# Kernel optimization log

Hardware: AMD Instinct MI355X
Metric: run time of the kernel (lower is better)

The kernel has to match this reference:

```python
import jax, jax.numpy as jnp
import numpy as np

B, S, D, H = 4, 1024, 1024, 16
HD = D // H
EPS = 1e-5


def layer_norm(x, scale, shift):
    mean = jnp.mean(x, axis=-1, keepdims=True)
    var = jnp.mean((x - mean) ** 2, axis=-1, keepdims=True)
    return scale * (x - mean) / jnp.sqrt(var + EPS) + shift


def gelu_tanh(x):
    c = jnp.sqrt(jnp.asarray(2.0 / jnp.pi, dtype=x.dtype))
    return 0.5 * x * (1.0 + jnp.tanh(c * (x + 0.044715 * x ** 3)))


def setup_inputs() -> dict:
    key = jax.random.key(0)
    ks = jax.random.split(key, 12)
    s = 0.02
    return {
        "x": jax.random.normal(ks[0], (B, S, D), dtype=jnp.float32),
        "attention_mask": jnp.ones((B, S), dtype=jnp.int32),
        "wq": jax.random.normal(ks[1], (D, D), dtype=jnp.float32) * s,
        "wk": jax.random.normal(ks[2], (D, D), dtype=jnp.float32) * s,
        "wv": jax.random.normal(ks[3], (D, D), dtype=jnp.float32) * s,
        "wo": jax.random.normal(ks[4], (D, D), dtype=jnp.float32) * s,
        "bo": jnp.zeros((D,), dtype=jnp.float32),
        "ln1_scale": jnp.ones((D,), dtype=jnp.float32),
        "ln1_shift": jnp.zeros((D,), dtype=jnp.float32),
        "ln2_scale": jnp.ones((D,), dtype=jnp.float32),
        "ln2_shift": jnp.zeros((D,), dtype=jnp.float32),
        "w1": jax.random.normal(ks[5], (D, 4 * D), dtype=jnp.float32) * s,
        "b1": jnp.zeros((4 * D,), dtype=jnp.float32),
        "w2": jax.random.normal(ks[6], (4 * D, D), dtype=jnp.float32) * s,
        "b2": jnp.zeros((D,), dtype=jnp.float32),
    }


def reference(x, attention_mask, wq, wk, wv, wo, bo, ln1_scale, ln1_shift,
              ln2_scale, ln2_shift, w1, b1, w2, b2):
    b, s, d = x.shape
    # --- pre-norm attention ---
    shortcut = x
    h = layer_norm(x, ln1_scale, ln1_shift)
    q = (h @ wq).reshape(b, s, H, HD).transpose(0, 2, 1, 3)  # bhsd
    k = (h @ wk).reshape(b, s, H, HD).transpose(0, 2, 1, 3)
    v = (h @ wv).reshape(b, s, H, HD).transpose(0, 2, 1, 3)
    scores = jnp.einsum('bhqd,bhkd->bhqk', q, k)
    causal = jnp.triu(jnp.ones((s, s), dtype=bool), k=1)  # True above diag -> masked
    neg_inf = jnp.asarray(-jnp.inf, dtype=scores.dtype)
    scores = jnp.where(causal, neg_inf, scores)
    pad = attention_mask[:, None, None, :].astype(bool)  # (b,1,1,k)
    scores = jnp.where(pad, scores, neg_inf)
    attn = jax.nn.softmax(scores / jnp.sqrt(jnp.asarray(HD, dtype=scores.dtype)), axis=-1)
    ctx = jnp.einsum('bhqk,bhkd->bhqd', attn, v)
    ctx = ctx.transpose(0, 2, 1, 3).reshape(b, s, d)
    x = shortcut + (ctx @ wo + bo)
    # --- pre-norm FFN ---
    shortcut = x
    h = layer_norm(x, ln2_scale, ln2_shift)
    h = gelu_tanh(h @ w1 + b1) @ w2 + b2
    return shortcut + h
```

## Files before the change

kernel.cpp:

```cpp
#include <hip/hip_runtime.h>
#include <hip/hip_bf16.h>
#include <math.h>

#define B_ 4
#define S_ 1024
#define D_ 1024
#define H_ 16
#define HD_ 64

typedef __hip_bfloat16 bf16_t;
typedef __attribute__((ext_vector_type(8))) short bf16x8;
typedef __attribute__((ext_vector_type(4))) float floatx4;

__device__ __forceinline__ float bf2f(ushort u) {
  return __uint_as_float((unsigned)u << 16);
}

__global__ __launch_bounds__(256) void prep_kernel(
    const float* __restrict__ x, const float* __restrict__ ln1s,
    const float* __restrict__ ln1b, bf16_t* __restrict__ h,
    const float* __restrict__ wq, const float* __restrict__ wk,
    const float* __restrict__ wv, const float* __restrict__ wo,
    const float* __restrict__ w1, const float* __restrict__ w2,
    bf16_t* __restrict__ wqkv_t, bf16_t* __restrict__ wo_t,
    bf16_t* __restrict__ w1_t, bf16_t* __restrict__ w2_t) {
  const int id = blockIdx.x;
  if (id < 4096) {
    const int row = id;
    float4 v = ((const float4*)(x + (size_t)row * D_))[threadIdx.x];
    float s = v.x + v.y + v.z + v.w;
    float ss = v.x * v.x + v.y * v.y + v.z * v.z + v.w * v.w;
#pragma unroll
    for (int off = 32; off > 0; off >>= 1) {
      s += __shfl_xor(s, off);
      ss += __shfl_xor(ss, off);
    }
    __shared__ float ls[4], lss[4], stats[2];
    const int wave = threadIdx.x >> 6, lane = threadIdx.x & 63;
    if (lane == 0) { ls[wave] = s; lss[wave] = ss; }
    __syncthreads();
    if (threadIdx.x == 0) {
      float t = ls[0] + ls[1] + ls[2] + ls[3];
      float tt = lss[0] + lss[1] + lss[2] + lss[3];
      float mean = t * (1.0f / D_);
      stats[0] = mean;
      stats[1] = rsqrtf(tt * (1.0f / D_) - mean * mean + 1e-5f);
    }
    __syncthreads();
    const float mean = stats[0], rstd = stats[1];
    float4 sc = ((const float4*)ln1s)[threadIdx.x];
    float4 sh = ((const float4*)ln1b)[threadIdx.x];
    bf16_t ob[4];
    ob[0] = __float2bfloat16(sc.x * (v.x - mean) * rstd + sh.x);
    ob[1] = __float2bfloat16(sc.y * (v.y - mean) * rstd + sh.y);
    ob[2] = __float2bfloat16(sc.z * (v.z - mean) * rstd + sh.z);
    ob[3] = __float2bfloat16(sc.w * (v.w - mean) * rstd + sh.w);
    *(ushort4*)(h + (size_t)row * D_ + threadIdx.x * 4) = *(ushort4*)ob;
    return;
  }
  const float* W;
  bf16_t* Wt;
  int K, N, n0, k0;
  if (id < 8192) {
    const int t = id - 4096, which = t >> 10, tile = t & 1023;
    n0 = (tile & 31) * 32;
    k0 = (tile >> 5) * 32;
    K = 1024; N = 1024;
    W = which == 0 ? wq : which == 1 ? wk : which == 2 ? wv : wo;
    Wt = which < 3 ? wqkv_t + (size_t)which * 1024 * 1024 : wo_t;
  } else if (id < 12288) {
    const int tile = id - 8192;
    n0 = (tile & 127) * 32;
    k0 = (tile >> 7) * 32;
    K = 1024; N = 4096;
    W = w1; Wt = w1_t;
  } else {
    const int tile = id - 12288;
    n0 = (tile & 31) * 32;
    k0 = (tile >> 5) * 32;
    K = 4096; N = 1024;
    W = w2; Wt = w2_t;
  }
  __shared__ float t[32][33];
  const int lx = threadIdx.x & 31, ly = threadIdx.x >> 5;
#pragma unroll
  for (int r = ly; r < 32; r += 8) t[r][lx] = W[(size_t)(k0 + r) * N + n0 + lx];
  __syncthreads();
#pragma unroll
  for (int r = ly; r < 32; r += 8)
    Wt[(size_t)(n0 + r) * K + k0 + lx] = __float2bfloat16(t[lx][r]);
}

__global__ __launch_bounds__(256) void mgemm_kernel(const bf16_t* __restrict__ A,
                                                    const bf16_t* __restrict__ Bt,
                                                    const float* __restrict__ bias,
                                                    void* __restrict__ C,
                                                    int M, int N, int K, int Kc,
                                                    int Mt, int Nt, int PM,
                                                    int mode) {
  __shared__ bf16_t As[128 * 64];
  __shared__ bf16_t Bs[128 * 64];
  const int tid = threadIdx.x;
  const int lane = tid & 63, w = tid >> 6;

  const int flat = blockIdx.x;
  const int xcd = flat & 7;
  int t0 = flat >> 3;
  const int mb = xcd % PM, nb = xcd / PM;
  const int mt = mb * Mt + (t0 % Mt);
  t0 /= Mt;
  const int nt = nb * Nt + (t0 % Nt);
  const int z = t0 / Nt;
  const int m0 = mt * 128, n0 = nt * 128;
  const int kz0 = z * Kc;
  const int wm = (w >> 1) * 64, wn = (w & 1) * 64;

  floatx4 zero = {0.f, 0.f, 0.f, 0.f};
  floatx4 acc[4][4];
#pragma unroll
  for (int i = 0; i < 4; i++)
#pragma unroll
    for (int j = 0; j < 4; j++) acc[i][j] = zero;

  const int ro8 = lane >> 3;
  const int g8 = ((lane & 7) ^ ro8) * 8;
  const bf16_t* ga[4];
  const bf16_t* gb[4];
  bf16_t* la[4];
  bf16_t* lb[4];
#pragma unroll
  for (int t = 0; t < 4; t++) {
    const int c = w + 4 * t;
    ga[t] = A + (size_t)(m0 + c * 8 + ro8) * K + g8;
    gb[t] = Bt + (size_t)(n0 + c * 8 + ro8) * K + g8;
    la[t] = &As[c * 512];
    lb[t] = &Bs[c * 512];
  }

  const int fr = lane & 15, quad = lane >> 4;

  for (int k0 = kz0; k0 < kz0 + Kc; k0 += 64) {
    __syncthreads();
#pragma unroll
    for (int t = 0; t < 4; t++) {
      __builtin_amdgcn_global_load_lds(
          (const __attribute__((address_space(1))) void*)(ga[t] + k0),
          (__attribute__((address_space(3))) void*)la[t], 16, 0, 0);
      __builtin_amdgcn_global_load_lds(
          (const __attribute__((address_space(1))) void*)(gb[t] + k0),
          (__attribute__((address_space(3))) void*)lb[t], 16, 0, 0);
    }
    __syncthreads();

#pragma unroll
    for (int ks = 0; ks < 2; ks++) {
      const int sq = ((quad + 4 * ks) ^ (fr & 7)) * 8;
      bf16x8 af[4], bfr[4];
#pragma unroll
      for (int i = 0; i < 4; i++) {
        af[i] = *(const bf16x8*)&As[(wm + i * 16 + fr) * 64 + sq];
        bfr[i] = *(const bf16x8*)&Bs[(wn + i * 16 + fr) * 64 + sq];
      }
#pragma unroll
      for (int i = 0; i < 4; i++)
#pragma unroll
        for (int j = 0; j < 4; j++)
          acc[i][j] = __builtin_amdgcn_mfma_f32_16x16x32_bf16(af[i], bfr[j],
                                                              acc[i][j], 0, 0, 0);
    }
  }

  bf16_t* Pz = (mode == 4) ? ((bf16_t*)C + (size_t)z * M * N) : nullptr;
#pragma unroll
  for (int j = 0; j < 4; j++) {
    const int col = n0 + wn + j * 16 + fr;
    const float bj = bias ? bias[col] : 0.f;
#pragma unroll
    for (int i = 0; i < 4; i++) {
      const int rbase = m0 + wm + i * 16 + quad * 4;
#pragma unroll
      for (int r = 0; r < 4; r++) {
        const int row = rbase + r;
        float c = acc[i][j][r] + bj;
        if (mode == 1) {
          const float xg = c;
          const float t = 0.7978845608028654f * (xg + 0.044715f * xg * xg * xg);
          const float th = 2.0f / (1.0f + __expf(-2.0f * t)) - 1.0f;
          c = 0.5f * xg * (1.0f + th);
        }
        if (mode == 4) {
          Pz[(size_t)row * N + col] = __float2bfloat16(c);
        } else {
          ((bf16_t*)C)[(size_t)row * N + col] = __float2bfloat16(c);
        }
      }
    }
  }
}

__global__ __launch_bounds__(512, 2) void mgemm256_kernel(
    const bf16_t* __restrict__ A, const bf16_t* __restrict__ Bt,
    const float* __restrict__ bias, void* __restrict__ C, int M, int N, int K,
    int Kc, int Mt, int Nt, int PM, int mode) {
  __shared__ bf16_t sm[65536];
  const int tid = threadIdx.x;
  const int lane = tid & 63, w = tid >> 6;

  const int flat = blockIdx.x;
  const int xcd = flat & 7;
  int t0 = flat >> 3;
  const int mb = xcd % PM, nb = xcd / PM;
  const int mt = mb * Mt + (t0 % Mt);
  t0 /= Mt;
  const int nt = nb * Nt + (t0 % Nt);
  const int z = t0 / Nt;
  const int m0 = mt * 256, n0 = nt * 256;
  const int kz0 = z * Kc;
  const int wr = w >> 2, wc = w & 3;

  floatx4 zero = {0.f, 0.f, 0.f, 0.f};
  floatx4 acc[8][4];
#pragma unroll
  for (int i = 0; i < 8; i++)
#pragma unroll
    for (int j = 0; j < 4; j++) acc[i][j] = zero;

  const int ro8 = lane >> 3;
  const int g8 = ((lane & 7) ^ ro8) * 8;
  const bf16_t* gA0 = A + (size_t)(m0 + w * 8 + ro8) * K + g8;
  const bf16_t* gB0 = Bt + (size_t)(n0 + w * 8 + ro8) * K + g8;

  auto STAGE = [&](int bufi, int mat, int half, int kk) {
    const bf16_t* g0 = (mat == 0) ? gA0 : gB0;
#pragma unroll
    for (int l = 0; l < 2; ++l) {
      const bf16_t* src = g0 + (size_t)(half * 128 + l * 64) * K + kk;
      __builtin_amdgcn_global_load_lds(
          (const __attribute__((address_space(1))) void*)src,
          (__attribute__((address_space(3))) void*)
              &sm[((bufi * 2 + mat) * 2 + half) * 8192 + (l * 8 + w) * 512],
          16, 0, 0);
    }
  };

  const int fr = lane & 15, quad = lane >> 4;
  const int ntk = Kc >> 6;

  STAGE(0, 0, 0, kz0); STAGE(0, 0, 1, kz0);
  STAGE(0, 1, 0, kz0); STAGE(0, 1, 1, kz0);
  asm volatile("s_waitcnt vmcnt(0)" ::: "memory");
  __builtin_amdgcn_s_barrier();

  for (int t = 0; t < ntk; ++t) {
    const int buf = t & 1, nbuf = buf ^ 1;
    const int kn = kz0 + (t + 1) * 64;
    const bool pre = (t + 1 < ntk);
#pragma unroll
    for (int p = 0; p < 4; ++p) {
      const int mh = p >> 1, jh = p & 1;
      bf16x8 af[2][4], bfr[2][2];
#pragma unroll
      for (int ks = 0; ks < 2; ++ks) {
        const int sq = ((quad + 4 * ks) ^ (fr & 7)) * 8;
#pragma unroll
        for (int i = 0; i < 4; ++i)
          af[ks][i] = *(const bf16x8*)&sm[((buf * 2 + 0) * 2 + wr) * 8192 +
                                          ((mh * 4 + i) * 16 + fr) * 64 + sq];
#pragma unroll
        for (int j = 0; j < 2; ++j)
          bfr[ks][j] =
              *(const bf16x8*)&sm[((buf * 2 + 1) * 2 + (wc >> 1)) * 8192 +
                                  ((wc & 1) * 64 + (jh * 2 + j) * 16 + fr) * 64 +
                                  sq];
      }
      if (p == 0 && pre) { STAGE(nbuf, 0, 0, kn); STAGE(nbuf, 0, 1, kn); }
      if (p == 1 && pre) { STAGE(nbuf, 1, 0, kn); STAGE(nbuf, 1, 1, kn); }
      asm volatile("s_waitcnt lgkmcnt(8)" ::: "memory");
      __builtin_amdgcn_s_barrier();
      asm volatile("s_waitcnt lgkmcnt(0)" ::: "memory");
      __builtin_amdgcn_sched_barrier(0);
      __builtin_amdgcn_s_setprio(1);
#pragma unroll
      for (int ks = 0; ks < 2; ++ks)
#pragma unroll
        for (int i = 0; i < 4; ++i)
#pragma unroll
          for (int j = 0; j < 2; ++j)
            acc[mh * 4 + i][jh * 2 + j] = __builtin_amdgcn_mfma_f32_16x16x32_bf16(
                af[ks][i], bfr[ks][j], acc[mh * 4 + i][jh * 2 + j], 0, 0, 0);
      __builtin_amdgcn_s_setprio(0);
      if (p == 3) asm volatile("s_waitcnt vmcnt(0)" ::: "memory");
      __builtin_amdgcn_s_barrier();
    }
  }

  __syncthreads();
  bf16_t* sl = sm + w * 8192;
  bf16_t* Pz = (mode == 4) ? ((bf16_t*)C + (size_t)z * M * N) : (bf16_t*)C;
  float bj[4];
#pragma unroll
  for (int j = 0; j < 4; ++j)
    bj[j] = bias ? bias[n0 + wc * 64 + j * 16 + fr] : 0.f;
#pragma unroll
  for (int i = 0; i < 8; ++i)
#pragma unroll
    for (int j = 0; j < 4; ++j)
#pragma unroll
      for (int r = 0; r < 4; ++r) {
        const int row = i * 16 + quad * 4 + r, col = j * 16 + fr;
        float c = acc[i][j][r] + bj[j];
        if (mode == 1) {
          const float xg = c;
          const float t2 = 0.7978845608028654f * (xg + 0.044715f * xg * xg * xg);
          const float th = 2.0f / (1.0f + __expf(-2.0f * t2)) - 1.0f;
          c = 0.5f * xg * (1.0f + th);
        }
        const int cg = (col >> 3) ^ (row & 7);
        sl[row * 64 + cg * 8 + (col & 7)] = __float2bfloat16(c);
      }
#pragma unroll
  for (int it = 0; it < 16; ++it) {
    const int gi = it * 64 + lane;
    const int row = gi >> 3, g = gi & 7;
    const bf16x8 vv = *(const bf16x8*)&sl[row * 64 + ((g ^ (row & 7)) * 8)];
    *(bf16x8*)&Pz[(size_t)(m0 + wr * 128 + row) * N + n0 + wc * 64 + g * 8] = vv;
  }
}

__global__ __launch_bounds__(256) void reduce2_ln_kernel(
    const bf16_t* __restrict__ P, size_t slice, const float* __restrict__ x,
    const float* __restrict__ bias, const float* __restrict__ scale,
    const float* __restrict__ shift, float* __restrict__ out,
    bf16_t* __restrict__ h) {
  const int row = blockIdx.x;
  const size_t e = (size_t)row * D_ + threadIdx.x * 4;
  const float4 xv = *(const float4*)(x + e);
  const ushort4 p0 = *(const ushort4*)((const ushort*)P + e);
  const ushort4 p1 = *(const ushort4*)((const ushort*)P + slice + e);
  const float4 bb = *(const float4*)(bias + threadIdx.x * 4);
  float4 v;
  v.x = xv.x + bf2f(p0.x) + bf2f(p1.x) + bb.x;
  v.y = xv.y + bf2f(p0.y) + bf2f(p1.y) + bb.y;
  v.z = xv.z + bf2f(p0.z) + bf2f(p1.z) + bb.z;
  v.w = xv.w + bf2f(p0.w) + bf2f(p1.w) + bb.w;
  *(float4*)(out + e) = v;

  float s = v.x + v.y + v.z + v.w;
  float ss = v.x * v.x + v.y * v.y + v.z * v.z + v.w * v.w;
#pragma unroll
  for (int off = 32; off > 0; off >>= 1) {
    s += __shfl_xor(s, off);
    ss += __shfl_xor(ss, off);
  }
  __shared__ float ls[4], lss[4], stats[2];
  const int wave = threadIdx.x >> 6, lane = threadIdx.x & 63;
  if (lane == 0) { ls[wave] = s; lss[wave] = ss; }
  __syncthreads();
  if (threadIdx.x == 0) {
    float t = ls[0] + ls[1] + ls[2] + ls[3];
    float tt = lss[0] + lss[1] + lss[2] + lss[3];
    float mean = t * (1.0f / D_);
    stats[0] = mean;
    stats[1] = rsqrtf(tt * (1.0f / D_) - mean * mean + 1e-5f);
  }
  __syncthreads();
  const float mean = stats[0], rstd = stats[1];
  const float4 sc = *(const float4*)(scale + threadIdx.x * 4);
  const float4 sh = *(const float4*)(shift + threadIdx.x * 4);
  bf16_t ob[4];
  ob[0] = __float2bfloat16(sc.x * (v.x - mean) * rstd + sh.x);
  ob[1] = __float2bfloat16(sc.y * (v.y - mean) * rstd + sh.y);
  ob[2] = __float2bfloat16(sc.z * (v.z - mean) * rstd + sh.z);
  ob[3] = __float2bfloat16(sc.w * (v.w - mean) * rstd + sh.w);
  *(ushort4*)(h + e) = *(ushort4*)ob;
}

__global__ __launch_bounds__(256) void reduce4_kernel(const bf16_t* __restrict__ P,
                                                      size_t slice,
                                                      const float* __restrict__ bias,
                                                      float* __restrict__ out,
                                                      int N) {
  const size_t e = ((size_t)blockIdx.x * 256 + threadIdx.x) * 4;
  const ushort* Pu = (const ushort*)P;
  const ushort4 p0 = *(const ushort4*)(Pu + e);
  const ushort4 p1 = *(const ushort4*)(Pu + slice + e);
  const ushort4 p2 = *(const ushort4*)(Pu + 2 * slice + e);
  const ushort4 p3 = *(const ushort4*)(Pu + 3 * slice + e);
  const float4 r = *(const float4*)(out + e);
  const float4 bb = *(const float4*)(bias + (int)(e % N));
  float4 o;
  o.x = r.x + bb.x + bf2f(p0.x) + bf2f(p1.x) + bf2f(p2.x) + bf2f(p3.x);
  o.y = r.y + bb.y + bf2f(p0.y) + bf2f(p1.y) + bf2f(p2.y) + bf2f(p3.y);
  o.z = r.z + bb.z + bf2f(p0.z) + bf2f(p1.z) + bf2f(p2.z) + bf2f(p3.z);
  o.w = r.w + bb.w + bf2f(p0.w) + bf2f(p1.w) + bf2f(p2.w) + bf2f(p3.w);
  *(float4*)(out + e) = o;
}

__global__ __launch_bounds__(256) void fattn_kernel(const bf16_t* __restrict__ QK,
                                                    const bf16_t* __restrict__ VT,
                                                    const int* __restrict__ mask,
                                                    bf16_t* __restrict__ O) {
  const int qt = gridDim.x - 1 - blockIdx.x;
  const int h = blockIdx.y, b = blockIdx.z;
  const int tid = threadIdx.x;
  const int lane = tid & 63, w = tid >> 6;
  const int tx = lane & 15, quad = lane >> 4;
  const int q0 = qt * 64;

  __shared__ bf16_t Ks[64 * 64];
  __shared__ bf16_t Vs[64 * 64];
  __shared__ ushort Ps[64 * 64];

  const int ro8 = lane >> 3;
  const int g8 = ((lane & 7) ^ ro8) * 8;
  const bf16_t* gk[2];
  const bf16_t* gv[2];
  bf16_t* lk[2];
  bf16_t* lv[2];
#pragma unroll
  for (int t = 0; t < 2; t++) {
    const int c = w + 4 * t;
    gk[t] = QK + (size_t)((size_t)b * S_ + c * 8 + ro8) * 2048 + 1024 + h * HD_ + g8;
    gv[t] = VT + (size_t)(h * HD_ + c * 8 + ro8) * 4096 + (size_t)b * S_ + g8;
    lk[t] = &Ks[c * 512];
    lv[t] = &Vs[c * 512];
  }

  bf16x8 qf[2];
#pragma unroll
  for (int ks = 0; ks < 2; ks++)
    qf[ks] = *(const bf16x8*)(QK + (size_t)((size_t)b * S_ + q0 + w * 16 + tx) * 2048 +
                              h * HD_ + ks * 32 + quad * 8);

  const short oneb = 0x3F80;
  bf16x8 vones = {oneb, oneb, oneb, oneb, oneb, oneb, oneb, oneb};

  floatx4 ctx[4], lacc;
#pragma unroll
  for (int nt = 0; nt < 4; nt++) {
    ctx[nt].x = 0.f; ctx[nt].y = 0.f; ctx[nt].z = 0.f; ctx[nt].w = 0.f;
  }
  lacc.x = 0.f; lacc.y = 0.f; lacc.z = 0.f; lacc.w = 0.f;

  for (int kt = 0; kt <= qt; kt++) {
    const int k0 = kt * 64;
    __syncthreads();
#pragma unroll
    for (int t = 0; t < 2; t++) {
      __builtin_amdgcn_global_load_lds(
          (const __attribute__((address_space(1))) void*)(gk[t] + (size_t)k0 * 2048),
          (__attribute__((address_space(3))) void*)lk[t], 16, 0, 0);
      __builtin_amdgcn_global_load_lds(
          (const __attribute__((address_space(1))) void*)(gv[t] + k0),
          (__attribute__((address_space(3))) void*)lv[t], 16, 0, 0);
    }
    __syncthreads();

    floatx4 accS[4];
#pragma unroll
    for (int nt = 0; nt < 4; nt++) {
      accS[nt].x = 0.f; accS[nt].y = 0.f; accS[nt].z = 0.f; accS[nt].w = 0.f;
    }
#pragma unroll
    for (int ks = 0; ks < 2; ks++) {
      const int sq = ((quad + 4 * ks) ^ (tx & 7)) * 8;
      bf16x8 kf[4];
#pragma unroll
      for (int nt = 0; nt < 4; nt++)
        kf[nt] = *(const bf16x8*)&Ks[(nt * 16 + tx) * 64 + sq];
#pragma unroll
      for (int nt = 0; nt < 4; nt++)
        accS[nt] = __builtin_amdgcn_mfma_f32_16x16x32_bf16(qf[ks], kf[nt],
                                                           accS[nt], 0, 0, 0);
    }

#pragma unroll
    for (int nt = 0; nt < 4; nt++) {
      const int jc = k0 + nt * 16 + tx;
      const bool ok = mask[b * S_ + jc] != 0;
      const int col = nt * 16 + tx;
#pragma unroll
      for (int r = 0; r < 4; r++) {
        const int qq = quad * 4 + r;
        const int qrow = q0 + w * 16 + qq;
        float p = exp2f(accS[nt][r] * 0.1803368801111244f);
        if (jc > qrow || !ok) p = 0.f;
        const int pc = ((((col >> 3) ^ (qq & 7)) << 3)) | (col & 7);
        Ps[(w * 16 + qq) * 64 + pc] =
            ((__hip_bfloat16_raw)__float2bfloat16(p)).x;
      }
    }

#pragma unroll
    for (int ks = 0; ks < 2; ks++) {
      const int sq = ((quad + 4 * ks) ^ (tx & 7)) * 8;
      const bf16x8 pf = *(const bf16x8*)&Ps[(w * 16 + tx) * 64 + sq];
      bf16x8 vf[4];
#pragma unroll
      for (int nt = 0; nt < 4; nt++)
        vf[nt] = *(const bf16x8*)&Vs[(nt * 16 + tx) * 64 + sq];
#pragma unroll
      for (int nt = 0; nt < 4; nt++)
        ctx[nt] = __builtin_amdgcn_mfma_f32_16x16x32_bf16(pf, vf[nt],
                                                          ctx[nt], 0, 0, 0);
      lacc = __builtin_amdgcn_mfma_f32_16x16x32_bf16(pf, vones, lacc, 0, 0, 0);
    }
  }

  const size_t obase = (size_t)b * S_ * D_ + (size_t)h * HD_;
  float rinv[4];
#pragma unroll
  for (int r = 0; r < 4; r++) rinv[r] = 1.0f / lacc[r];
#pragma unroll
  for (int nt = 0; nt < 4; nt++)
#pragma unroll
    for (int r = 0; r < 4; r++) {
      const int q = q0 + w * 16 + quad * 4 + r;
      O[obase + (size_t)q * D_ + nt * 16 + tx] =
          __float2bfloat16(ctx[nt][r] * rinv[r]);
    }
}

extern "C" void kernel_launch(void* const* d_in, const int* in_sizes, int n_in,
                              void* d_out, int out_size, void* d_ws, size_t ws_size,
                              hipStream_t stream) {
  const float* x = (const float*)d_in[0];
  const int* mask = (const int*)d_in[1];
  const float* wq = (const float*)d_in[2];
  const float* wk = (const float*)d_in[3];
  const float* wv = (const float*)d_in[4];
  const float* wo = (const float*)d_in[5];
  const float* bo = (const float*)d_in[6];
  const float* ln2s = (const float*)d_in[9];
  const float* ln2b = (const float*)d_in[10];
  const float* w1 = (const float*)d_in[11];
  const float* b1 = (const float*)d_in[12];
  const float* w2 = (const float*)d_in[13];
  const float* b2 = (const float*)d_in[14];
  float* out = (float*)d_out;

  const int M = B_ * S_;
  char* ws = (char*)d_ws;
  const size_t MB = (size_t)1 << 20;
  bf16_t* qk = (bf16_t*)(ws);
  bf16_t* vT = (bf16_t*)(ws + 16 * MB);
  bf16_t* ffn1 = (bf16_t*)(ws);
  bf16_t* ctx = (bf16_t*)(ws + 32 * MB);
  bf16_t* h = (bf16_t*)(ws + 40 * MB);
  bf16_t* wqkv_t = (bf16_t*)(ws + 48 * MB);
  bf16_t* wo_t = (bf16_t*)(ws + 54 * MB);
  bf16_t* w1_t = (bf16_t*)(ws + 56 * MB);
  bf16_t* w2_t = (bf16_t*)(ws + 64 * MB);
  bf16_t* Pa = (bf16_t*)(ws);
  bf16_t* Pf = (bf16_t*)(ws + 32 * MB);
  const size_t slice = (size_t)M * D_;

  prep_kernel<<<dim3(16384), 256, 0, stream>>>(x, (const float*)d_in[7],
                                               (const float*)d_in[8], h, wq, wk,
                                               wv, wo, w1, w2, wqkv_t, wo_t,
                                               w1_t, w2_t);

  mgemm_kernel<<<dim3(16 * 32), 256, 0, stream>>>(
      h, wqkv_t, nullptr, qk, M, 2 * D_, D_, D_, 8, 8, 4, 0);

  mgemm_kernel<<<dim3(8 * 32), 256, 0, stream>>>(
      wqkv_t + (size_t)2 * 1024 * 1024, h, nullptr, vT, D_, M, D_, D_,
      4, 8, 2, 0);

  fattn_kernel<<<dim3(S_ / 64, H_, B_), 256, 0, stream>>>(qk, vT, mask, ctx);

  mgemm_kernel<<<dim3(8 * 32 * 2), 256, 0, stream>>>(
      ctx, wo_t, nullptr, Pa, M, D_, D_, D_ / 2, 4, 8, 8, 4);

  reduce2_ln_kernel<<<dim3(M), 256, 0, stream>>>(Pa, slice, x, bo, ln2s, ln2b,
                                                 out, h);

  mgemm256_kernel<<<dim3(256), 512, 0, stream>>>(
      h, w1_t, b1, ffn1, M, 4 * D_, D_, D_, 4, 8, 4, 1);

  mgemm256_kernel<<<dim3(256), 512, 0, stream>>>(
      ffn1, w2_t, nullptr, Pf, M, D_, 4 * D_, D_, 2, 4, 8, 4);

  reduce4_kernel<<<dim3((size_t)M * D_ / 1024), 256, 0, stream>>>(
      Pf, slice, b2, out, D_);
}
```

Before: 354.1 us.

## Use four-stage LDS ring with K=32 tiles and single barrier per step

Replaces the double-buffered K=64 GEMM main loop, which used four sub-phases and multiple barriers per step, with a four-buffer ring of K=32 tiles prefetched three steps ahead. Each step waits on a vmcnt count and issues one barrier, then loads all fragments and runs 32 MFMAs. Staging is reorganized so each thread loads one row segment with a 4-way XOR swizzle. The aim is to hide global-to-LDS latency and cut barrier overhead. The price is smaller MFMA work per step and the risk of a race on ring-buffer reuse, since there is only one barrier per iteration.

Result: no change. 355.5 us (+0.4%).

```diff
diff --git a/kernel.cpp b/kernel.cpp
--- a/kernel.cpp
+++ b/kernel.cpp
@@ -225,73 +225,70 @@
 #pragma unroll
     for (int j = 0; j < 4; j++) acc[i][j] = zero;
 
-  const int ro8 = lane >> 3;
-  const int g8 = ((lane & 7) ^ ro8) * 8;
-  const bf16_t* gA0 = A + (size_t)(m0 + w * 8 + ro8) * K + g8;
-  const bf16_t* gB0 = Bt + (size_t)(n0 + w * 8 + ro8) * K + g8;
-
-  auto STAGE = [&](int bufi, int mat, int half, int kk) {
-    const bf16_t* g0 = (mat == 0) ? gA0 : gB0;
+  const int r0 = tid >> 2;
+  const int gx = (((tid & 3) ^ (r0 & 3)) << 3);
+  const bf16_t* gA0 = A + (size_t)(m0 + r0) * K + gx;
+  const bf16_t* gB0 = Bt + (size_t)(n0 + r0) * K + gx;
+  const int dstE = tid * 8;
+
+  auto STAGE = [&](int bufi, int kk) {
 #pragma unroll
     for (int l = 0; l < 2; ++l) {
-      const bf16_t* src = g0 + (size_t)(half * 128 + l * 64) * K + kk;
       __builtin_amdgcn_global_load_lds(
-          (const __attribute__((address_space(1))) void*)src,
-          (__attribute__((address_space(3))) void*)
-              &sm[((bufi * 2 + mat) * 2 + half) * 8192 + (l * 8 + w) * 512],
+          (const __attribute__((address_space(1))) void*)(gA0 +
+                                                          (size_t)l * 128 * K + kk),
+          (__attribute__((address_space(3))) void*)&sm[bufi * 16384 + l * 4096 +
+                                                       dstE],
           16, 0, 0);
+      __builtin_amdgcn_global_load_lds(
+          (const __attribute__((address_space(1))) void*)(gB0 +
+                                                          (size_t)l * 128 * K + kk),
+          (__attribute__((address_space(3))) void*)&sm[bufi * 16384 + 8192 +
+                                                       l * 4096 + dstE],
+          16, 0, 0);
     }
   };
 
   const int fr = lane & 15, quad = lane >> 4;
-  const int ntk = Kc >> 6;
-
-  STAGE(0, 0, 0, kz0); STAGE(0, 0, 1, kz0);
-  STAGE(0, 1, 0, kz0); STAGE(0, 1, 1, kz0);
-  asm volatile("s_waitcnt vmcnt(0)" ::: "memory");
-  __builtin_amdgcn_s_barrier();
+  const int ntk = Kc >> 5;
+
+  STAGE(0, kz0);
+  STAGE(1, kz0 + 32);
+  STAGE(2, kz0 + 64);
 
   for (int t = 0; t < ntk; ++t) {
-    const int buf = t & 1, nbuf = buf ^ 1;
-    const int kn = kz0 + (t + 1) * 64;
-    const bool pre = (t + 1 < ntk);
-#pragma unroll
-    for (int p = 0; p < 4; ++p) {
-      const int mh = p >> 1, jh = p & 1;
-      bf16x8 af[2][4], bfr[2][2];
-#pragma unroll
-      for (int ks = 0; ks < 2; ++ks) {
-        const int sq = ((quad + 4 * ks) ^ (fr & 7)) * 8;
-#pragma unroll
-        for (int i = 0; i < 4; ++i)
-          af[ks][i] = *(const bf16x8*)&sm[((buf * 2 + 0) * 2 + wr) * 8192 +
-                                          ((mh * 4 + i) * 16 + fr) * 64 + sq];
-#pragma unroll
-        for (int j = 0; j < 2; ++j)
-          bfr[ks][j] =
-              *(const bf16x8*)&sm[((buf * 2 + 1) * 2 + (wc >> 1)) * 8192 +
-                                  ((wc & 1) * 64 + (jh * 2 + j) * 16 + fr) * 64 +
-                                  sq];
-      }
-      if (p == 0 && pre) { STAGE(nbuf, 0, 0, kn); STAGE(nbuf, 0, 1, kn); }
-      if (p == 1 && pre) { STAGE(nbuf, 1, 0, kn); STAGE(nbuf, 1, 1, kn); }
-      asm volatile("s_waitcnt lgkmcnt(8)" ::: "memory");
-      __builtin_amdgcn_s_barrier();
-      asm volatile("s_waitcnt lgkmcnt(0)" ::: "memory");
-      __builtin_amdgcn_sched_barrier(0);
-      __builtin_amdgcn_s_setprio(1);
-#pragma unroll
-      for (int ks = 0; ks < 2; ++ks)
-#pragma unroll
-        for (int i = 0; i < 4; ++i)
-#pragma unroll
-          for (int j = 0; j < 2; ++j)
-            acc[mh * 4 + i][jh * 2 + j] = __builtin_amdgcn_mfma_f32_16x16x32_bf16(
-                af[ks][i], bfr[ks][j], acc[mh * 4 + i][jh * 2 + j], 0, 0, 0);
-      __builtin_amdgcn_s_setprio(0);
-      if (p == 3) asm volatile("s_waitcnt vmcnt(0)" ::: "memory");
-      __builtin_amdgcn_s_barrier();
-    }
+    if (t + 2 < ntk) {
+      asm volatile("s_waitcnt vmcnt(8)" ::: "memory");
+    } else if (t + 1 < ntk) {
+      asm volatile("s_waitcnt vmcnt(4)" ::: "memory");
+    } else {
+      asm volatile("s_waitcnt vmcnt(0)" ::: "memory");
+    }
+    __builtin_amdgcn_s_barrier();
+
+    const int bb = (t & 3) * 16384;
+    bf16x8 af[8], bfr[4];
+#pragma unroll
+    for (int i = 0; i < 8; ++i) {
+      const int row = wr * 128 + i * 16 + fr;
+      af[i] = *(const bf16x8*)&sm[bb + row * 32 + ((quad ^ (fr & 3)) << 3)];
+    }
+#pragma unroll
+    for (int j = 0; j < 4; ++j) {
+      const int row = wc * 64 + j * 16 + fr;
+      bfr[j] = *(const bf16x8*)&sm[bb + 8192 + row * 32 +
+                                   ((quad ^ (fr & 3)) << 3)];
+    }
+    if (t + 3 < ntk) STAGE((t + 3) & 3, kz0 + (t + 3) * 32);
+
+    __builtin_amdgcn_s_setprio(1);
+#pragma unroll
+    for (int i = 0; i < 8; ++i)
+#pragma unroll
+      for (int j = 0; j < 4; ++j)
+        acc[i][j] = __builtin_amdgcn_mfma_f32_16x16x32_bf16(af[i], bfr[j],
+                                                            acc[i][j], 0, 0, 0);
+    __builtin_amdgcn_s_setprio(0);
   }
 
   __syncthreads();
```

## Restructure 256x256 GEMM main loop into four per-unit phases with finer prefetch

Applied to the files above, without the earlier changes.

Rewrites the mgemm256 main loop so each k-tile runs as four phases, indexed by k-half and M-half. Each phase issues one staging unit of the next tile via global_load_lds and waits with vmcnt(2) instead of draining all loads. B fragments are loaded once per k-half and reused across both M-halves. Launch bounds drop from 2 to 1 block per CU, which loosens register pressure at the cost of occupancy, and the epilogue is split into two M-halves with smaller per-wave LDS staging.

Result: faster. 345.2 us (-2.5%).

```diff
diff --git a/kernel.cpp b/kernel.cpp
--- a/kernel.cpp
+++ b/kernel.cpp
@@ -198,7 +198,7 @@
   }
 }
 
-__global__ __launch_bounds__(512, 2) void mgemm256_kernel(
+__global__ __launch_bounds__(512, 1) void mgemm256_kernel(
     const bf16_t* __restrict__ A, const bf16_t* __restrict__ Bt,
     const float* __restrict__ bias, void* __restrict__ C, int M, int N, int K,
     int Kc, int Mt, int Nt, int PM, int mode) {
@@ -216,7 +216,7 @@
   const int z = t0 / Nt;
   const int m0 = mt * 256, n0 = nt * 256;
   const int kz0 = z * Kc;
-  const int wr = w >> 2, wc = w & 3;
+  const int wr = (w >> 2) & 1, wc = w & 3;
 
   floatx4 zero = {0.f, 0.f, 0.f, 0.f};
   floatx4 acc[8][4];
@@ -225,105 +225,112 @@
 #pragma unroll
     for (int j = 0; j < 4; j++) acc[i][j] = zero;
 
-  const int ro8 = lane >> 3;
-  const int g8 = ((lane & 7) ^ ro8) * 8;
-  const bf16_t* gA0 = A + (size_t)(m0 + w * 8 + ro8) * K + g8;
-  const bf16_t* gB0 = Bt + (size_t)(n0 + w * 8 + ro8) * K + g8;
-
-  auto STAGE = [&](int bufi, int mat, int half, int kk) {
-    const bf16_t* g0 = (mat == 0) ? gA0 : gB0;
+  const int r_t = tid >> 3;
+  const int g8s = (((tid & 7) ^ (r_t & 7)) << 3);
+  const int fr = lane & 15, quad = lane >> 4;
+
+  auto STAGE = [&](int nbuf, int unit, int kk) {
+    const bf16_t* src0 =
+        (unit < 2) ? Bt + (size_t)(n0 + (unit & 1) * 128 + r_t) * K + g8s + kk
+                   : A + (size_t)(m0 + (unit & 1) * 128 + r_t) * K + g8s + kk;
+    bf16_t* d0 = &sm[nbuf * 32768 + (unit < 2 ? 16384 : 0) + (unit & 1) * 8192 +
+                     tid * 8];
 #pragma unroll
     for (int l = 0; l < 2; ++l) {
-      const bf16_t* src = g0 + (size_t)(half * 128 + l * 64) * K + kk;
       __builtin_amdgcn_global_load_lds(
-          (const __attribute__((address_space(1))) void*)src,
-          (__attribute__((address_space(3))) void*)
-              &sm[((bufi * 2 + mat) * 2 + half) * 8192 + (l * 8 + w) * 512],
-          16, 0, 0);
+          (const __attribute__((address_space(1))) void*)(src0 +
+                                                          (size_t)l * 64 * K),
+          (__attribute__((address_space(3))) void*)(d0 + l * 4096), 16, 0, 0);
     }
   };
 
-  const int fr = lane & 15, quad = lane >> 4;
   const int ntk = Kc >> 6;
 
-  STAGE(0, 0, 0, kz0); STAGE(0, 0, 1, kz0);
-  STAGE(0, 1, 0, kz0); STAGE(0, 1, 1, kz0);
-  asm volatile("s_waitcnt vmcnt(0)" ::: "memory");
+  STAGE(0, 0, kz0); STAGE(0, 1, kz0); STAGE(0, 2, kz0); STAGE(0, 3, kz0);
+  asm volatile("s_waitcnt vmcnt(2)" ::: "memory");
   __builtin_amdgcn_s_barrier();
 
+#define DO_PHASE(KS, MH, UNIT)                                                 \
+  {                                                                            \
+    const int sq = (((quad + 4 * (KS)) ^ (fr & 7)) << 3);                      \
+    bf16x8 af[4];                                                              \
+    _Pragma("unroll") for (int i = 0; i < 4; ++i) af[i] =                      \
+        *(const bf16x8*)&sm[bo + ((MH)*128 + wr * 64 + i * 16 + fr) * 64 + sq];\
+    if ((MH) == 0) {                                                           \
+      _Pragma("unroll") for (int j = 0; j < 4; ++j) bfr[j] =                   \
+          *(const bf16x8*)&sm[bo + 16384 + (wc * 64 + j * 16 + fr) * 64 + sq]; \
+    }                                                                          \
+    if (pre) STAGE(nbuf, (UNIT), kn);                                          \
+    __builtin_amdgcn_s_barrier();                                              \
+    asm volatile("s_waitcnt lgkmcnt(0)" ::: "memory");                         \
+    __builtin_amdgcn_sched_barrier(0);                                         \
+    __builtin_amdgcn_s_setprio(1);                                             \
+    _Pragma("unroll") for (int i = 0; i < 4; ++i)                              \
+        _Pragma("unroll") for (int j = 0; j < 4; ++j) acc[(MH)*4 + i][j] =     \
+            __builtin_amdgcn_mfma_f32_16x16x32_bf16(af[i], bfr[j],             \
+                                                    acc[(MH)*4 + i][j], 0, 0,  \
+                                                    0);                        \
+    __builtin_amdgcn_s_setprio(0);                                             \
+    if (pre) {                                                                 \
+      asm volatile("s_waitcnt vmcnt(2)" ::: "memory");                         \
+    } else {                                                                   \
+      asm volatile("s_waitcnt vmcnt(0)" ::: "memory");                         \
+    }                                                                          \
+    __builtin_amdgcn_s_barrier();                                              \
+  }
+
   for (int t = 0; t < ntk; ++t) {
-    const int buf = t & 1, nbuf = buf ^ 1;
+    const int bo = (t & 1) * 32768;
+    const int nbuf = (t + 1) & 1;
     const int kn = kz0 + (t + 1) * 64;
     const bool pre = (t + 1 < ntk);
-#pragma unroll
-    for (int p = 0; p < 4; ++p) {
-      const int mh = p >> 1, jh = p & 1;
-      bf16x8 af[2][4], bfr[2][2];
-#pragma unroll
-      for (int ks = 0; ks < 2; ++ks) {
-        const int sq = ((quad + 4 * ks) ^ (fr & 7)) * 8;
-#pragma unroll
-        for (int i = 0; i < 4; ++i)
-          af[ks][i] = *(const bf16x8*)&sm[((buf * 2 + 0) * 2 + wr) * 8192 +
-                                          ((mh * 4 + i) * 16 + fr) * 64 + sq];
-#pragma unroll
-        for (int j = 0; j < 2; ++j)
-          bfr[ks][j] =
-              *(const bf16x8*)&sm[((buf * 2 + 1) * 2 + (wc >> 1)) * 8192 +
-                                  ((wc & 1) * 64 + (jh * 2 + j) * 16 + fr) * 64 +
-                                  sq];
-      }
-      if (p == 0 && pre) { STAGE(nbuf, 0, 0, kn); STAGE(nbuf, 0, 1, kn); }
-      if (p == 1 && pre) { STAGE(nbuf, 1, 0, kn); STAGE(nbuf, 1, 1, kn); }
-      asm volatile("s_waitcnt lgkmcnt(8)" ::: "memory");
-      __builtin_amdgcn_s_barrier();
+    bf16x8 bfr[4];
+    DO_PHASE(0, 0, 0)
+    DO_PHASE(0, 1, 1)
+    DO_PHASE(1, 0, 2)
+    DO_PHASE(1, 1, 3)
+  }
+#undef DO_PHASE
+
+  __syncthreads();
+  bf16_t* sl = sm + w * 4096;
+  bf16_t* Pz = (mode == 4) ? ((bf16_t*)C + (size_t)z * M * N) : (bf16_t*)C;
+  float bj[4];
+#pragma unroll
+  for (int j = 0; j < 4; ++j)
+    bj[j] = bias ? bias[n0 + wc * 64 + j * 16 + fr] : 0.f;
+#pragma unroll
+  for (int mh = 0; mh < 2; ++mh) {
+    if (mh) {
       asm volatile("s_waitcnt lgkmcnt(0)" ::: "memory");
       __builtin_amdgcn_sched_barrier(0);
-      __builtin_amdgcn_s_setprio(1);
-#pragma unroll
-      for (int ks = 0; ks < 2; ++ks)
-#pragma unroll
-        for (int i = 0; i < 4; ++i)
-#pragma unroll
-          for (int j = 0; j < 2; ++j)
-            acc[mh * 4 + i][jh * 2 + j] = __builtin_amdgcn_mfma_f32_16x16x32_bf16(
-                af[ks][i], bfr[ks][j], acc[mh * 4 + i][jh * 2 + j], 0, 0, 0);
-      __builtin_amdgcn_s_setprio(0);
-      if (p == 3) asm volatile("s_waitcnt vmcnt(0)" ::: "memory");
-      __builtin_amdgcn_s_barrier();
-    }
-  }
-
-  __syncthreads();
-  bf16_t* sl = sm + w * 8192;
-  bf16_t* Pz = (mode == 4) ? ((bf16_t*)C + (size_t)z * M * N) : (bf16_t*)C;
-  float bj[4];
-#pragma unroll
-  for (int j = 0; j < 4; ++j)
-    bj[j] = bias ? bias[n0 + wc * 64 + j * 16 + fr] : 0.f;
-#pragma unroll
-  for (int i = 0; i < 8; ++i)
-#pragma unroll
-    for (int j = 0; j < 4; ++j)
-#pragma unroll
-      for (int r = 0; r < 4; ++r) {
-        const int row = i * 16 + quad * 4 + r, col = j * 16 + fr;
-        float c = acc[i][j][r] + bj[j];
-        if (mode == 1) {
-          const float xg = c;
-          const float t2 = 0.7978845608028654f * (xg + 0.044715f * xg * xg * xg);
-          const float th = 2.0f / (1.0f + __expf(-2.0f * t2)) - 1.0f;
-          c = 0.5f * xg * (1.0f + th);
+    }
+#pragma unroll
+    for (int i = 0; i < 4; ++i)
+#pragma unroll
+      for (int j = 0; j < 4; ++j)
+#pragma unroll
+        for (int r = 0; r < 4; ++r) {
+          const int rl = i * 16 + quad * 4 + r, cl = j * 16 + fr;
+          float c = acc[mh * 4 + i][j][r] + bj[j];
+          if (mode == 1) {
+            const float xg = c;
+            const float t2 =
+                0.7978845608028654f * (xg + 0.044715f * xg * xg * xg);
+            const float th = 2.0f / (1.0f + __expf(-2.0f * t2)) - 1.0f;
+            c = 0.5f * xg * (1.0f + th);
+          }
+          const int cg = (cl >> 3) ^ (rl & 7);
+          sl[rl * 64 + cg * 8 + (cl & 7)] = __float2bfloat16(c);
         }
-        const int cg = (col >> 3) ^ (row & 7);
-        sl[row * 64 + cg * 8 + (col & 7)] = __float2bfloat16(c);
-      }
-#pragma unroll
-  for (int it = 0; it < 16; ++it) {
-    const int gi = it * 64 + lane;
-    const int row = gi >> 3, g = gi & 7;
-    const bf16x8 vv = *(const bf16x8*)&sl[row * 64 + ((g ^ (row & 7)) * 8)];
-    *(bf16x8*)&Pz[(size_t)(m0 + wr * 128 + row) * N + n0 + wc * 64 + g * 8] = vv;
+#pragma unroll
+    for (int it = 0; it < 8; ++it) {
+      const int gi = it * 64 + lane;
+      const int rl = gi >> 3, g = gi & 7;
+      const bf16x8 vv = *(const bf16x8*)&sl[rl * 64 + ((g ^ (rl & 7)) * 8)];
+      *(bf16x8*)&Pz[(size_t)(m0 + mh * 128 + wr * 64 + rl) * N + n0 + wc * 64 +
+                    g * 8] = vv;
+    }
   }
 }
 
```
